# Performance work log

Hardware: AMD Instinct MI355X
Metric: run time of the kernel (lower is better)

## Reference

```python
import jax, jax.numpy as jnp
import numpy as np

# SDNet-CTRL cfg constants
MU = 0.1          # FISTA step size (cfg['MODEL']['MU'])
LMBD = 0.1        # sparsity weight (cfg['MODEL']['LAMBDA'][0])
N_STEPS = 4       # FISTA iterations (cfg['MODEL']['NUM_LAYERS'])
EPS_BN = 1e-5


def _conv(x, w, stride, padding):
    # torch F.conv2d, NCHW / OIHW
    return jax.lax.conv_general_dilated(
        x, w, window_strides=(stride, stride),
        padding=[(padding, padding), (padding, padding)],
        dimension_numbers=('NCHW', 'OIHW', 'NCHW'))


def _conv_t(c, w, stride, padding):
    # torch F.conv_transpose2d(c, w, stride, padding) with output_padding chosen
    # so that it exactly inverts the spatial map of _conv (k=4,s=2,p=1 -> 0).
    k = w.shape[2]
    w_t = jnp.flip(w, (2, 3)).transpose(1, 0, 2, 3)  # (I,O,k,k) flipped
    pad = k - 1 - padding
    return jax.lax.conv_general_dilated(
        c, w_t, window_strides=(1, 1),
        padding=[(pad, pad), (pad, pad)],
        lhs_dilation=(stride, stride),
        dimension_numbers=('NCHW', 'OIHW', 'NCHW'))


def _shrink_nn(c, thr):
    # non-negative soft threshold (cfg NONEGATIVE=True)
    return jax.nn.relu(c - thr)


def _dict_conv(x, w, stride, padding):
    # DictBlock: FISTA convolutional sparse coding, n_dict=1, w_norm=True.
    # normalize each dictionary atom (output filter) to unit l2 norm
    wn = w * jax.lax.rsqrt(jnp.sum(w * w, axis=(1, 2, 3), keepdims=True))
    ss = MU
    thr = LMBD * ss
    # t = 0
    c = _shrink_nn(ss * _conv(x, wn, stride, padding), thr)
    c_pre_pre = jnp.zeros_like(c)
    c_pre = c
    tk = 1.0
    for t in range(1, N_STEPS):
        tk_pre = tk
        tk = (1.0 + float(np.sqrt(1.0 + 4.0 * tk_pre * tk_pre))) / 2.0
        y = c_pre + ((tk_pre - 1.0) / tk) * (c_pre - c_pre_pre)
        r = x - _conv_t(y, wn, stride, padding)      # residual in image space
        c = _shrink_nn(y + ss * _conv(r, wn, stride, padding), thr)
        c_pre_pre, c_pre = c_pre, c
    return c


def _bn(x, g, b):
    # training-mode BatchNorm2d (batch statistics)
    m = jnp.mean(x, axis=(0, 2, 3), keepdims=True)
    v = jnp.var(x, axis=(0, 2, 3), keepdims=True)
    return g.reshape(1, -1, 1, 1) * (x - m) * jax.lax.rsqrt(v + EPS_BN) + b.reshape(1, -1, 1, 1)


def _lrelu(x):
    return jnp.where(x >= 0, x, 0.2 * x)


def setup_inputs() -> dict:
    key = jax.random.key(0)
    ks = jax.random.split(key, 5)
    nc, ndf, nz = 3, 128, 256
    B, H = 256, 32

    def mk_w(k, o, i):
        return jax.random.normal(k, (o, i, 4, 4), jnp.float32) * 0.02

    return {
        'x': jax.random.normal(ks[0], (B, nc, H, H), jnp.float32),
        'w1': mk_w(ks[1], ndf, nc),
        'w2': mk_w(ks[2], 2 * ndf, ndf),
        'w3': mk_w(ks[3], 4 * ndf, 2 * ndf),
        'w4': mk_w(ks[4], nz, 4 * ndf),
        'g2': jnp.ones((2 * ndf,), jnp.float32),
        'b2': jnp.zeros((2 * ndf,), jnp.float32),
        'g3': jnp.ones((4 * ndf,), jnp.float32),
        'b3': jnp.zeros((4 * ndf,), jnp.float32),
    }


def reference(x, w1, w2, w3, w4, g2, b2, g3, b3):
    h = _lrelu(_dict_conv(x, w1, 2, 1))                 # (B, ndf, 16, 16)
    h = _lrelu(_bn(_dict_conv(h, w2, 2, 1), g2, b2))    # (B, 2ndf, 8, 8)
    h = _lrelu(_bn(_dict_conv(h, w3, 2, 1), g3, b3))    # (B, 4ndf, 4, 4)
    h = _dict_conv(h, w4, 1, 0)                         # (B, nz, 1, 1)
    h = h.reshape(h.shape[0], -1)                       # Flatten
    n = jnp.sqrt(jnp.sum(h * h, axis=1, keepdims=True))
    return h / jnp.maximum(n, 1e-12)                    # F.normalize(dim=1)
```

## Files before the change

kernel.cpp:

```cpp
#include <hip/hip_runtime.h>
#include <math.h>

#define SS   0.1f
#define THRC 0.01f

typedef __attribute__((ext_vector_type(8))) short s16x8;
typedef __attribute__((ext_vector_type(4))) float f32x4;

__device__ __forceinline__ float b2f(unsigned short u){
  union{unsigned int i; float f;} v; v.i = ((unsigned int)u)<<16; return v.f;
}
__device__ __forceinline__ unsigned short f2b(float f){
  union{float f; unsigned int i;} v; v.f = f;
  return (unsigned short)((v.i + 0x7fffu + ((v.i>>16)&1u))>>16);
}
__device__ __forceinline__ s16x8 as_s16x8(uint4 u){
  union{uint4 a; s16x8 b;} c; c.a = u; return c.b;
}
__device__ __forceinline__ int swz8(int row, int q){ return (row<<3) | (q ^ (row&7)); }

__device__ __forceinline__ void gld16(const void* g, void* l){
  __builtin_amdgcn_global_load_lds(
      (const __attribute__((address_space(1))) unsigned int*)g,
      (__attribute__((address_space(3))) unsigned int*)l, 16, 0, 0);
}

enum { EPI_FIRST=0, EPI_UPDATE=1, EPI_PARTIAL=2, EPI_RES_NHWC=3, EPI_RES_FLAT=4 };

struct EpiM {
  unsigned short* C;
  const unsigned short* Y;
  const unsigned short* Cprev;
  unsigned short* Yout;
  const unsigned short* img;
  const unsigned short* zp;
  float coef;
  int lH, lW, lC;
  int S_MN, Kc;
};

struct LA_ident {
  const unsigned short* A; int K;
  __device__ void setz(int){}
  __device__ __forceinline__ const unsigned short* addr(int m, int k8) const {
    return A + (size_t)m*K + ((size_t)k8<<3);
  }
};
struct LA_nhwc {
  const unsigned short* img; const unsigned short* zp; int lH, lW, lC;
  __device__ void setz(int){}
  __device__ __forceinline__ const unsigned short* addr(int m, int k8) const {
    int lWo = lW-1, lHo = lH-1;
    int wo = m & ((1<<lWo)-1); int t = m>>lWo; int ho = t & ((1<<lHo)-1); int b = t>>lHo;
    int k = k8<<3; int kk = k>>lC; int i = k & ((1<<lC)-1);
    int kw = kk&3, kh = kk>>2;
    int h = 2*ho + kh - 1, w = 2*wo + kw - 1;
    if ((unsigned)h >= (1u<<lH) || (unsigned)w >= (1u<<lW)) return zp;
    return img + (((((((size_t)b<<lH)|h)<<lW)|w))<<lC) + i;
  }
};
struct LA_yg {
  const unsigned short* y; const unsigned short* zp; int lHo, lWo, lO, ph, pw;
  __device__ void setz(int z){ ph = z>>1; pw = z&1; }
  __device__ __forceinline__ const unsigned short* addr(int m, int k8) const {
    int l = m & ((1<<lWo)-1); int t = m>>lWo; int j = t & ((1<<lHo)-1); int b = t>>lHo;
    int k = k8<<3; int tt = k>>lO; int o = k & ((1<<lO)-1);
    int th = tt>>1, tw = tt&1;
    int ho = ph ? (j+1-th) : (j-th);
    int wo = pw ? (l+1-tw) : (l-tw);
    if ((unsigned)ho >= (1u<<lHo) || (unsigned)wo >= (1u<<lWo)) return zp;
    return y + (((((((size_t)b<<lHo)|ho)<<lWo)|wo))<<lO) + o;
  }
};
struct LA_padb {
  const unsigned short* img;
  __device__ void setz(int){}
  __device__ __forceinline__ const unsigned short* addr(int m, int k8) const {
    int wo = m&15, t = m>>4, ho = t&15, b = t>>4;
    int kh = k8>>1, kw0 = (k8&1)<<1;
    int h = 2*ho + kh, w = 2*wo + kw0;
    return img + (((size_t)b*34 + h)*34 + w)*4;
  }
};

template<class AL, int EPI>
__global__ __launch_bounds__(512)
void mgemm_k(AL al, const unsigned short* __restrict__ Bw, int M, int N, int K, EpiM ep)
{
  __shared__ uint4 S[2][2048];
  const int tid = threadIdx.x;
  const int bm = blockIdx.y<<7, bn = blockIdx.x<<7;
  const int z = blockIdx.z;
  int kb = 0, ke = K;
  const unsigned short* Bp = Bw;
  if (EPI == EPI_PARTIAL){ kb = z*ep.Kc; ke = kb + ep.Kc; }
  if (EPI == EPI_RES_NHWC){ Bp = Bw + (size_t)z*(size_t)N*K; al.setz(z); }

  f32x4 acc[4][2];
  #pragma unroll
  for (int i=0;i<4;++i)
    #pragma unroll
    for (int j=0;j<2;++j){ acc[i][j][0]=0.f; acc[i][j][1]=0.f; acc[i][j][2]=0.f; acc[i][j][3]=0.f; }

  const int lane = tid & 63, wid = tid >> 6;
  const int wm = (wid>>2)<<6, wn = (wid&3)<<5;
  const int fr = lane & 15, fq = lane >> 4;

  auto issue = [&](int k0, int b){
    int k8 = k0>>3;
    #pragma unroll
    for (int i=0;i<2;++i){
      int s  = (wid<<7) + (i<<6) + lane;
      int sr = s>>3, q = (s&7) ^ (sr&7);
      gld16(al.addr(bm+sr, k8+q), (void*)&S[b][(wid<<7) + (i<<6)]);
    }
    #pragma unroll
    for (int i=0;i<2;++i){
      int s  = (wid<<7) + (i<<6) + lane;
      int sr = s>>3, q = (s&7) ^ (sr&7);
      int gn = bn + sr;
      const unsigned short* src = (gn < N) ? Bp + (size_t)gn*K + ((size_t)(k8+q)<<3) : ep.zp;
      gld16(src, (void*)&S[b][1024 + (wid<<7) + (i<<6)]);
    }
  };

  issue(kb, 0);
  int buf = 0;
  for (int k0 = kb; k0 < ke; k0 += 64){
    asm volatile("s_waitcnt vmcnt(0)" ::: "memory");
    __builtin_amdgcn_s_barrier();
    __builtin_amdgcn_sched_barrier(0);
    if (k0 + 64 < ke) issue(k0 + 64, buf^1);
    const uint4* As = &S[buf][0];
    const uint4* Bs = &S[buf][1024];
    #pragma unroll
    for (int half=0; half<2; ++half){
      const int qb = (half<<2) | fq;
      s16x8 af[4], bf[2];
      #pragma unroll
      for (int mi=0;mi<4;++mi) af[mi] = as_s16x8(As[swz8(wm + mi*16 + fr, qb)]);
      #pragma unroll
      for (int ni=0;ni<2;++ni) bf[ni] = as_s16x8(Bs[swz8(wn + ni*16 + fr, qb)]);
      #pragma unroll
      for (int mi=0;mi<4;++mi)
        #pragma unroll
        for (int ni=0;ni<2;++ni)
          acc[mi][ni] = __builtin_amdgcn_mfma_f32_16x16x32_bf16(af[mi], bf[ni], acc[mi][ni], 0,0,0);
    }
    buf ^= 1;
  }

  #pragma unroll
  for (int mi=0;mi<4;++mi){
    #pragma unroll
    for (int ni=0;ni<2;++ni){
      int n = bn + wn + ni*16 + fr;
      if (n >= N) continue;
      int mb = bm + wm + mi*16 + (fq<<2);
      #pragma unroll
      for (int r=0;r<4;++r){
        int m = mb + r;
        float a = acc[mi][ni][r];
        if (EPI == EPI_FIRST){
          float v = SS*a - THRC; v = v>0.f ? v : 0.f;
          ep.C[(size_t)m*N + n] = f2b(v);
        } else if (EPI == EPI_UPDATE){
          size_t idx = (size_t)m*N + n;
          float v = b2f(ep.Y[idx]) + SS*a - THRC; v = v>0.f ? v : 0.f;
          ep.C[idx] = f2b(v);
          if (ep.Yout) ep.Yout[idx] = f2b(v + ep.coef*(v - b2f(ep.Cprev[idx])));
        } else if (EPI == EPI_PARTIAL){
          ep.C[(size_t)z*ep.S_MN + (size_t)m*N + n] = f2b(a);
        } else if (EPI == EPI_RES_NHWC){
          int lWo = ep.lW-1, lHo = ep.lH-1;
          int l = m & ((1<<lWo)-1); int t = m>>lWo; int j = t & ((1<<lHo)-1); int b = t>>lHo;
          int h = 2*j + (z>>1), w = 2*l + (z&1);
          size_t ridx = (((((((size_t)b<<ep.lH)|h)<<ep.lW)|w))<<ep.lC) | n;
          ep.C[ridx] = f2b(b2f(ep.img[ridx]) - a);
        } else {
          size_t ridx = (size_t)m*N + n;
          ep.C[ridx] = f2b(b2f(ep.img[ridx]) - a);
        }
      }
    }
  }
}

__global__ __launch_bounds__(64)
void wnorm1_k(const float* __restrict__ w, unsigned short* __restrict__ wf1,
              unsigned short* __restrict__ wcolT)
{
  int o = blockIdx.x, tid = threadIdx.x;
  __shared__ float red[64];
  float v = (tid < 48) ? w[(size_t)o*48 + tid] : 0.f;
  red[tid] = v*v; __syncthreads();
  for (int d=32; d>0; d>>=1){ if (tid<d) red[tid] += red[tid+d]; __syncthreads(); }
  float nv = v * rsqrtf(red[0]);
  if (tid < 48){
    int c = tid>>4, t = tid&15;
    wf1[(size_t)o*64 + t*4 + c] = f2b(nv);
    wcolT[(size_t)(t*4+c)*128 + o] = f2b(nv);
  } else {
    int t = tid - 48;
    wf1[(size_t)o*64 + t*4 + 3] = 0;
    wcolT[(size_t)(t*4+3)*128 + o] = 0;
  }
}
__global__ __launch_bounds__(256)
void wnormX_k(const float* __restrict__ w, int Cin, int O,
              unsigned short* __restrict__ wT, unsigned short* __restrict__ wclsT,
              unsigned short* __restrict__ wEO)
{
  int o = blockIdx.x, tid = threadIdx.x; int E = Cin*16;
  __shared__ float red[256];
  float s = 0.f;
  for (int e = tid; e < E; e += 256){ float v = w[(size_t)o*E + e]; s += v*v; }
  red[tid] = s; __syncthreads();
  for (int d=128; d>0; d>>=1){ if (tid<d) red[tid] += red[tid+d]; __syncthreads(); }
  float scale = rsqrtf(red[0]);
  for (int e = tid; e < E; e += 256){
    float v = w[(size_t)o*E + e] * scale;
    int i = e>>4, t = e&15, kh = t>>2, kw = t&3;
    int ee = t*Cin + i;
    if (wT)  wT[(size_t)o*E + ee] = f2b(v);
    if (wEO) wEO[(size_t)ee*O + o] = f2b(v);
    if (wclsT){
      int ph = (kh&1)^1, pw = (kw&1)^1, cls = ph*2+pw;
      int tt = (kh>>1)*2 + (kw>>1);
      wclsT[(((size_t)cls*Cin + i)*4 + tt)*O + o] = f2b(v);
    }
  }
}

__global__ void splitk_shrink_k(const unsigned short* __restrict__ part,
                                const unsigned short* __restrict__ Y,
                                unsigned short* __restrict__ C,
                                unsigned short* __restrict__ Yout,
                                const unsigned short* __restrict__ Cprev,
                                float coef, int MN, int S)
{
  for (int i = blockIdx.x*blockDim.x + threadIdx.x; i < MN; i += gridDim.x*blockDim.x){
    float s = 0.f;
    for (int zz = 0; zz < S; ++zz) s += b2f(part[(size_t)zz*MN + i]);
    float v = (Y ? b2f(Y[i]) : 0.f) + SS*s - THRC; v = v>0.f ? v : 0.f;
    C[i] = f2b(v);
    if (Yout) Yout[i] = f2b(v + coef*(v - b2f(Cprev[i])));
  }
}

__global__ void pad_x_k(const float* __restrict__ x, unsigned short* __restrict__ xpb){
  int idx = blockIdx.x*256 + threadIdx.x;
  if (idx >= 262144) return;
  int w = idx&31, t = idx>>5, h = t&31, b = t>>5;
  size_t src = (size_t)b*3072 + h*32 + w;
  unsigned short* d = xpb + (((size_t)b*34 + h+1)*34 + w+1)*4;
  d[0] = f2b(x[src]); d[1] = f2b(x[src+1024]); d[2] = f2b(x[src+2048]); d[3] = 0;
}

__global__ void l1_resid_k(const unsigned short* __restrict__ Col,
                           const float* __restrict__ x, unsigned short* __restrict__ r1pb)
{
  int idx = blockIdx.x*256 + threadIdx.x;
  if (idx >= 262144) return;
  int w = idx&31, t = idx>>5, h = t&31, b = t>>5;
  float a0=0.f, a1=0.f, a2=0.f;
  #pragma unroll
  for (int kh=0; kh<4; ++kh){
    int hh = h+1-kh; if (hh & 1) continue; int ho = hh>>1; if ((unsigned)ho >= 16u) continue;
    #pragma unroll
    for (int kw=0; kw<4; ++kw){
      int ww = w+1-kw; if (ww & 1) continue; int wo = ww>>1; if ((unsigned)wo >= 16u) continue;
      int m = (b*16+ho)*16+wo;
      const unsigned short* cp = Col + (size_t)m*64 + (kh*4+kw)*4;
      a0 += b2f(cp[0]); a1 += b2f(cp[1]); a2 += b2f(cp[2]);
    }
  }
  size_t src = (size_t)b*3072 + h*32 + w;
  unsigned short* d = r1pb + (((size_t)b*34 + h+1)*34 + w+1)*4;
  d[0] = f2b(x[src] - a0); d[1] = f2b(x[src+1024] - a1); d[2] = f2b(x[src+2048] - a2); d[3] = 0;
}

__global__ void bn_stats_k(const unsigned short* __restrict__ d, float* __restrict__ sums,
                           int rows, int O){
  for (int c = threadIdx.x; c < O; c += blockDim.x){
    float a = 0.f, b = 0.f;
    for (int r = blockIdx.x; r < rows; r += gridDim.x){
      float v = b2f(d[(size_t)r*O + c]); a += v; b += v*v;
    }
    atomicAdd(&sums[c], a); atomicAdd(&sums[O+c], b);
  }
}
__global__ void bn_apply_k(const unsigned short* __restrict__ d, const float* __restrict__ sums,
                           const float* __restrict__ g, const float* __restrict__ bta,
                           unsigned short* __restrict__ outp, int rows, int O, float inv_cnt){
  int total = rows*O;
  for (int i = blockIdx.x*blockDim.x + threadIdx.x; i < total; i += gridDim.x*blockDim.x){
    int c = i % O;
    float mean = sums[c]*inv_cnt;
    float var  = sums[O+c]*inv_cnt - mean*mean;
    float v = g[c]*(b2f(d[i])-mean)*rsqrtf(var + 1e-5f) + bta[c];
    outp[i] = f2b(v >= 0.f ? v : 0.2f*v);
  }
}

__global__ __launch_bounds__(256)
void norm_rows_k(const unsigned short* __restrict__ h, float* __restrict__ out){
  int row = blockIdx.x, tid = threadIdx.x;
  __shared__ float red[256];
  float v = b2f(h[(size_t)row*256 + tid]);
  red[tid] = v*v; __syncthreads();
  for (int d=128; d>0; d>>=1){ if (tid<d) red[tid] += red[tid+d]; __syncthreads(); }
  float nrm = sqrtf(red[0]); nrm = nrm > 1e-12f ? nrm : 1e-12f;
  out[(size_t)row*256 + tid] = v / nrm;
}

extern "C" void kernel_launch(void* const* d_in, const int* in_sizes, int n_in,
                              void* d_out, int out_size, void* d_ws, size_t ws_size,
                              hipStream_t stream)
{
  const float* x  = (const float*)d_in[0];
  const float* w1 = (const float*)d_in[1];
  const float* w2 = (const float*)d_in[2];
  const float* w3 = (const float*)d_in[3];
  const float* w4 = (const float*)d_in[4];
  const float* g2 = (const float*)d_in[5];
  const float* b2 = (const float*)d_in[6];
  const float* g3 = (const float*)d_in[7];
  const float* b3 = (const float*)d_in[8];
  float* out = (float*)d_out;

  char* p = (char*)d_ws;
  auto ah = [&](size_t n){ unsigned short* r = (unsigned short*)p; p += n*2; return r; };
  auto af = [&](size_t n){ float* r = (float*)p; p += n*4; return r; };

  unsigned short* wf1    = ah(128*64);
  unsigned short* wcol1T = ah(64*128);
  unsigned short* wT2    = ah((size_t)256*2048);
  unsigned short* wcls2  = ah((size_t)4*128*1024);
  unsigned short* wT3    = ah((size_t)512*4096);
  unsigned short* wcls3  = ah((size_t)4*256*2048);
  unsigned short* wT4    = ah((size_t)256*8192);
  unsigned short* wE4    = ah((size_t)8192*256);
  unsigned short* h1     = ah((size_t)8388608);
  unsigned short* h2     = ah((size_t)4194304);
  unsigned short* h3     = ah((size_t)2097152);
  unsigned short* cA     = ah((size_t)8388608);
  unsigned short* cB     = ah((size_t)8388608);
  unsigned short* yA     = ah((size_t)8388608);
  unsigned short* yB     = ah((size_t)8388608);
  unsigned short* rH     = ah((size_t)8388608);
  char* regionA = p; p += 17858560;
  unsigned short* Col    = (unsigned short*)regionA;
  unsigned short* xpb    = (unsigned short*)(regionA + 8388608);
  unsigned short* r1pb   = (unsigned short*)(regionA + 8388608 + 2367488);
  unsigned short* partL3 = (unsigned short*)regionA;
  unsigned short* partL4 = (unsigned short*)regionA;
  float* bnsum = af(1024);
  unsigned short* zp16 = ah(128);

  double tk = 1.0; float coef[4] = {0.f,0.f,0.f,0.f};
  for (int t = 1; t < 4; ++t){
    double tkp = tk; tk = (1.0 + sqrt(1.0 + 4.0*tkp*tkp))*0.5;
    coef[t] = (float)((tkp - 1.0)/tk);
  }

  hipMemsetAsync(zp16, 0, 256, stream);
  hipMemsetAsync(xpb,  0, 2367488, stream);
  hipMemsetAsync(r1pb, 0, 2367488, stream);
  pad_x_k<<<1024,256,0,stream>>>(x, xpb);
  wnorm1_k<<<128, 64, 0, stream>>>(w1, wf1, wcol1T);
  wnormX_k<<<256,256,0,stream>>>(w2, 128, 256, wT2, wcls2, nullptr);
  wnormX_k<<<512,256,0,stream>>>(w3, 256, 512, wT3, wcls3, nullptr);
  wnormX_k<<<256,256,0,stream>>>(w4, 512, 256, wT4, nullptr, wE4);

  auto l1_fwd = [&](const unsigned short* src, const unsigned short* Y, const unsigned short* Cp,
                    unsigned short* Cout, unsigned short* Yout, float cf){
    LA_padb al{src};
    EpiM ep{}; ep.C=Cout; ep.Y=Y; ep.Cprev=Cp; ep.Yout=Yout; ep.coef=cf; ep.zp=zp16;
    dim3 g(1, 512, 1);
    if (Y) mgemm_k<LA_padb,EPI_UPDATE><<<g,512,0,stream>>>(al, wf1, 65536,128,64, ep);
    else   mgemm_k<LA_padb,EPI_FIRST ><<<g,512,0,stream>>>(al, wf1, 65536,128,64, ep);
  };
  auto l1_tconv = [&](const unsigned short* y){
    LA_ident al{y, 128};
    EpiM ep{}; ep.C=Col; ep.S_MN=0; ep.Kc=128; ep.zp=zp16;
    mgemm_k<LA_ident,EPI_PARTIAL><<<dim3(1,512,1),512,0,stream>>>(al, wcol1T, 65536,64,128, ep);
    l1_resid_k<<<1024,256,0,stream>>>(Col, x, r1pb);
  };
  l1_fwd(xpb,  nullptr, nullptr, cA, nullptr, 0.f);
  l1_tconv(cA);
  l1_fwd(r1pb, cA, cA, cB, yA, coef[2]);
  l1_tconv(yA);
  l1_fwd(r1pb, yA, cB, cA, yB, coef[3]);
  l1_tconv(yB);
  l1_fwd(r1pb, yB, nullptr, h1, nullptr, 0.f);

  auto l2_fwd = [&](const unsigned short* src, const unsigned short* Y, const unsigned short* Cp,
                    unsigned short* Cout, unsigned short* Yout, float cf){
    LA_nhwc al{src, zp16, 4,4,7};
    EpiM ep{}; ep.C=Cout; ep.Y=Y; ep.Cprev=Cp; ep.Yout=Yout; ep.coef=cf; ep.zp=zp16;
    dim3 g(2, 128, 1);
    if (Y) mgemm_k<LA_nhwc,EPI_UPDATE><<<g,512,0,stream>>>(al, wT2, 16384,256,2048, ep);
    else   mgemm_k<LA_nhwc,EPI_FIRST ><<<g,512,0,stream>>>(al, wT2, 16384,256,2048, ep);
  };
  auto l2_tconv = [&](const unsigned short* y){
    LA_yg al{y, zp16, 3,3,8, 0,0};
    EpiM ep{}; ep.C=rH; ep.img=h1; ep.lH=4; ep.lW=4; ep.lC=7; ep.zp=zp16;
    mgemm_k<LA_yg,EPI_RES_NHWC><<<dim3(1,128,4),512,0,stream>>>(al, wcls2, 16384,128,1024, ep);
  };
  l2_fwd(h1, nullptr, nullptr, cA, nullptr, 0.f);
  l2_tconv(cA);
  l2_fwd(rH, cA, cA, cB, yA, coef[2]);
  l2_tconv(yA);
  l2_fwd(rH, yA, cB, cA, yB, coef[3]);
  l2_tconv(yB);
  l2_fwd(rH, yB, nullptr, cB, nullptr, 0.f);
  hipMemsetAsync(bnsum, 0, 2*256*sizeof(float), stream);
  bn_stats_k<<<256,256,0,stream>>>(cB, bnsum, 16384, 256);
  bn_apply_k<<<2048,256,0,stream>>>(cB, bnsum, g2, b2, h2, 16384, 256, 1.f/16384.f);

  auto l3_fwd = [&](const unsigned short* src, const unsigned short* Y, const unsigned short* Cp,
                    unsigned short* Cout, unsigned short* Yout, float cf){
    LA_nhwc al{src, zp16, 3,3,8};
    EpiM ep{}; ep.C=partL3; ep.S_MN=4096*512; ep.Kc=1024; ep.zp=zp16;
    mgemm_k<LA_nhwc,EPI_PARTIAL><<<dim3(4,32,4),512,0,stream>>>(al, wT3, 4096,512,4096, ep);
    splitk_shrink_k<<<1024,256,0,stream>>>(partL3, Y, Cout, Yout, Cp, cf, 4096*512, 4);
  };
  auto l3_tconv = [&](const unsigned short* y){
    LA_yg al{y, zp16, 2,2,9, 0,0};
    EpiM ep{}; ep.C=rH; ep.img=h2; ep.lH=3; ep.lW=3; ep.lC=8; ep.zp=zp16;
    mgemm_k<LA_yg,EPI_RES_NHWC><<<dim3(2,32,4),512,0,stream>>>(al, wcls3, 4096,256,2048, ep);
  };
  l3_fwd(h2, nullptr, nullptr, cA, nullptr, 0.f);
  l3_tconv(cA);
  l3_fwd(rH, cA, cA, cB, yA, coef[2]);
  l3_tconv(yA);
  l3_fwd(rH, yA, cB, cA, yB, coef[3]);
  l3_tconv(yB);
  l3_fwd(rH, yB, nullptr, cB, nullptr, 0.f);
  hipMemsetAsync(bnsum, 0, 2*512*sizeof(float), stream);
  bn_stats_k<<<256,256,0,stream>>>(cB, bnsum, 4096, 512);
  bn_apply_k<<<2048,256,0,stream>>>(cB, bnsum, g3, b3, h3, 4096, 512, 1.f/4096.f);

  auto l4_fwd = [&](const unsigned short* Asrc, const unsigned short* Y, const unsigned short* Cp,
                    unsigned short* Cout, unsigned short* Yout, float cf){
    LA_ident al{Asrc, 8192};
    EpiM ep{}; ep.C=partL4; ep.S_MN=65536; ep.Kc=256; ep.zp=zp16;
    mgemm_k<LA_ident,EPI_PARTIAL><<<dim3(2,2,32),512,0,stream>>>(al, wT4, 256,256,8192, ep);
    splitk_shrink_k<<<256,256,0,stream>>>(partL4, Y, Cout, Yout, Cp, cf, 65536, 32);
  };
  auto l4_tconv = [&](const unsigned short* y){
    LA_ident al{y, 256};
    EpiM ep{}; ep.C=rH; ep.img=h3; ep.zp=zp16;
    mgemm_k<LA_ident,EPI_RES_FLAT><<<dim3(64,2,1),512,0,stream>>>(al, wE4, 256,8192,256, ep);
  };
  l4_fwd(h3, nullptr, nullptr, cA, nullptr, 0.f);
  l4_tconv(cA);
  l4_fwd(rH, cA, cA, cB, yA, coef[2]);
  l4_tconv(yA);
  l4_fwd(rH, yA, cB, cA, yB, coef[3]);
  l4_tconv(yB);
  l4_fwd(rH, yB, nullptr, cB, nullptr, 0.f);

  norm_rows_k<<<256,256,0,stream>>>(cB, out);
}
```

Measured before the change: 889.3 us.

## Split-K layers 2-3 forward and transposed convs, single-buffer LDS, vectorize reductions

Moves the layer-2 forward GEMM and the layer-2/3 transposed-conv GEMMs to split-K with bf16 partial buffers, adds a tcomb kernel to reduce them and subtract from the image, and deepens split-K for layers 3 and 4. The GEMM kernel drops double-buffered LDS for a single buffer with load-then-barrier, halving LDS per block to raise occupancy at the cost of losing load/compute overlap. The split-K shrink reduction is vectorized to 16-byte loads. The aim is more blocks for small grids on many CUs, paid for with extra partial-sum memory traffic, extra launches, and bf16 rounding of partials.

```diff
diff --git a/kernel.cpp b/kernel.cpp
--- a/kernel.cpp
+++ b/kernel.cpp
@@ -25,7 +25,7 @@
       (__attribute__((address_space(3))) unsigned int*)l, 16, 0, 0);
 }
 
-enum { EPI_FIRST=0, EPI_UPDATE=1, EPI_PARTIAL=2, EPI_RES_NHWC=3, EPI_RES_FLAT=4 };
+enum { EPI_FIRST=0, EPI_UPDATE=1, EPI_PARTIAL=2, EPI_TPART=3, EPI_RES_FLAT=4 };
 
 struct EpiM {
   unsigned short* C;
@@ -35,8 +35,7 @@
   const unsigned short* img;
   const unsigned short* zp;
   float coef;
-  int lH, lW, lC;
-  int S_MN, Kc;
+  int S_MN, Kc, lgS;
 };
 
 struct LA_ident {
@@ -87,14 +86,19 @@
 __global__ __launch_bounds__(512)
 void mgemm_k(AL al, const unsigned short* __restrict__ Bw, int M, int N, int K, EpiM ep)
 {
-  __shared__ uint4 S[2][2048];
+  __shared__ uint4 As[1024];
+  __shared__ uint4 Bs[1024];
   const int tid = threadIdx.x;
   const int bm = blockIdx.y<<7, bn = blockIdx.x<<7;
   const int z = blockIdx.z;
   int kb = 0, ke = K;
   const unsigned short* Bp = Bw;
   if (EPI == EPI_PARTIAL){ kb = z*ep.Kc; ke = kb + ep.Kc; }
-  if (EPI == EPI_RES_NHWC){ Bp = Bw + (size_t)z*(size_t)N*K; al.setz(z); }
+  if (EPI == EPI_TPART){
+    int cls = z >> ep.lgS, kz = z & ((1<<ep.lgS)-1);
+    Bp = Bw + (size_t)cls*(size_t)N*K; al.setz(cls);
+    kb = kz*ep.Kc; ke = kb + ep.Kc;
+  }
 
   f32x4 acc[4][2];
   #pragma unroll
@@ -106,33 +110,32 @@
   const int wm = (wid>>2)<<6, wn = (wid&3)<<5;
   const int fr = lane & 15, fq = lane >> 4;
 
-  auto issue = [&](int k0, int b){
+  auto issueA = [&](int k0){
     int k8 = k0>>3;
     #pragma unroll
     for (int i=0;i<2;++i){
       int s  = (wid<<7) + (i<<6) + lane;
       int sr = s>>3, q = (s&7) ^ (sr&7);
-      gld16(al.addr(bm+sr, k8+q), (void*)&S[b][(wid<<7) + (i<<6)]);
-    }
+      gld16(al.addr(bm+sr, k8+q), (void*)&As[(wid<<7) + (i<<6)]);
+    }
+  };
+  auto issueB = [&](int k0){
+    int k8 = k0>>3;
     #pragma unroll
     for (int i=0;i<2;++i){
       int s  = (wid<<7) + (i<<6) + lane;
       int sr = s>>3, q = (s&7) ^ (sr&7);
       int gn = bn + sr;
       const unsigned short* src = (gn < N) ? Bp + (size_t)gn*K + ((size_t)(k8+q)<<3) : ep.zp;
-      gld16(src, (void*)&S[b][1024 + (wid<<7) + (i<<6)]);
-    }
-  };
-
-  issue(kb, 0);
-  int buf = 0;
+      gld16(src, (void*)&Bs[(wid<<7) + (i<<6)]);
+    }
+  };
+
   for (int k0 = kb; k0 < ke; k0 += 64){
+    issueA(k0); issueB(k0);
     asm volatile("s_waitcnt vmcnt(0)" ::: "memory");
     __builtin_amdgcn_s_barrier();
     __builtin_amdgcn_sched_barrier(0);
-    if (k0 + 64 < ke) issue(k0 + 64, buf^1);
-    const uint4* As = &S[buf][0];
-    const uint4* Bs = &S[buf][1024];
     #pragma unroll
     for (int half=0; half<2; ++half){
       const int qb = (half<<2) | fq;
@@ -147,7 +150,10 @@
         for (int ni=0;ni<2;++ni)
           acc[mi][ni] = __builtin_amdgcn_mfma_f32_16x16x32_bf16(af[mi], bf[ni], acc[mi][ni], 0,0,0);
     }
-    buf ^= 1;
+    if (k0 + 64 < ke){
+      __builtin_amdgcn_s_barrier();
+      __builtin_amdgcn_sched_barrier(0);
+    }
   }
 
   #pragma unroll
@@ -169,14 +175,8 @@
           float v = b2f(ep.Y[idx]) + SS*a - THRC; v = v>0.f ? v : 0.f;
           ep.C[idx] = f2b(v);
           if (ep.Yout) ep.Yout[idx] = f2b(v + ep.coef*(v - b2f(ep.Cprev[idx])));
-        } else if (EPI == EPI_PARTIAL){
+        } else if (EPI == EPI_PARTIAL || EPI == EPI_TPART){
           ep.C[(size_t)z*ep.S_MN + (size_t)m*N + n] = f2b(a);
-        } else if (EPI == EPI_RES_NHWC){
-          int lWo = ep.lW-1, lHo = ep.lH-1;
-          int l = m & ((1<<lWo)-1); int t = m>>lWo; int j = t & ((1<<lHo)-1); int b = t>>lHo;
-          int h = 2*j + (z>>1), w = 2*l + (z&1);
-          size_t ridx = (((((((size_t)b<<ep.lH)|h)<<ep.lW)|w))<<ep.lC) | n;
-          ep.C[ridx] = f2b(b2f(ep.img[ridx]) - a);
         } else {
           size_t ridx = (size_t)m*N + n;
           ep.C[ridx] = f2b(b2f(ep.img[ridx]) - a);
@@ -239,12 +239,65 @@
                                 const unsigned short* __restrict__ Cprev,
                                 float coef, int MN, int S)
 {
-  for (int i = blockIdx.x*blockDim.x + threadIdx.x; i < MN; i += gridDim.x*blockDim.x){
-    float s = 0.f;
-    for (int zz = 0; zz < S; ++zz) s += b2f(part[(size_t)zz*MN + i]);
-    float v = (Y ? b2f(Y[i]) : 0.f) + SS*s - THRC; v = v>0.f ? v : 0.f;
-    C[i] = f2b(v);
-    if (Yout) Yout[i] = f2b(v + coef*(v - b2f(Cprev[i])));
+  int total8 = MN>>3;
+  for (int i8 = blockIdx.x*blockDim.x + threadIdx.x; i8 < total8; i8 += gridDim.x*blockDim.x){
+    size_t off = (size_t)i8<<3;
+    float s[8];
+    #pragma unroll
+    for (int j=0;j<8;++j) s[j]=0.f;
+    for (int zz = 0; zz < S; ++zz){
+      uint4 pv = *(const uint4*)(part + (size_t)zz*MN + off);
+      const unsigned short* pe = (const unsigned short*)&pv;
+      #pragma unroll
+      for (int j=0;j<8;++j) s[j] += b2f(pe[j]);
+    }
+    uint4 yv = make_uint4(0,0,0,0), cp = make_uint4(0,0,0,0);
+    if (Y)    yv = *(const uint4*)(Y + off);
+    if (Yout) cp = *(const uint4*)(Cprev + off);
+    const unsigned short* ye = (const unsigned short*)&yv;
+    const unsigned short* ce = (const unsigned short*)&cp;
+    unsigned short co[8], yo[8];
+    #pragma unroll
+    for (int j=0;j<8;++j){
+      float v = (Y ? b2f(ye[j]) : 0.f) + SS*s[j] - THRC; v = v>0.f ? v : 0.f;
+      co[j] = f2b(v);
+      if (Yout) yo[j] = f2b(v + coef*(v - b2f(ce[j])));
+    }
+    *(uint4*)(C + off) = *(const uint4*)co;
+    if (Yout) *(uint4*)(Yout + off) = *(const uint4*)yo;
+  }
+}
+
+__global__ void tcomb_k(const unsigned short* __restrict__ part,
+                        const unsigned short* __restrict__ img,
+                        unsigned short* __restrict__ outp,
+                        int lH, int lW, int lC, int S, int MN, int total8)
+{
+  for (int i8 = blockIdx.x*blockDim.x + threadIdx.x; i8 < total8; i8 += gridDim.x*blockDim.x){
+    size_t idx = (size_t)i8<<3;
+    int c = (int)(idx & ((1u<<lC)-1));
+    int w = (int)(idx>>lC) & ((1<<lW)-1);
+    int h = (int)(idx>>(lC+lW)) & ((1<<lH)-1);
+    int b = (int)(idx>>(lC+lW+lH));
+    int j = h>>1, l = w>>1, cls = ((h&1)<<1)|(w&1);
+    int m = (((b<<(lH-1))|j)<<(lW-1))|l;
+    int N = 1<<lC;
+    const unsigned short* pb = part + ((size_t)cls*S)*MN + (size_t)m*N + c;
+    float s[8];
+    #pragma unroll
+    for (int q=0;q<8;++q) s[q]=0.f;
+    for (int kz=0; kz<S; ++kz){
+      uint4 pv = *(const uint4*)(pb + (size_t)kz*MN);
+      const unsigned short* pe = (const unsigned short*)&pv;
+      #pragma unroll
+      for (int q=0;q<8;++q) s[q] += b2f(pe[q]);
+    }
+    uint4 iv = *(const uint4*)(img + idx);
+    const unsigned short* ie = (const unsigned short*)&iv;
+    unsigned short ro[8];
+    #pragma unroll
+    for (int q=0;q<8;++q) ro[q] = f2b(b2f(ie[q]) - s[q]);
+    *(uint4*)(outp + idx) = *(const uint4*)ro;
   }
 }
 
@@ -349,12 +402,11 @@
   unsigned short* yA     = ah((size_t)8388608);
   unsigned short* yB     = ah((size_t)8388608);
   unsigned short* rH     = ah((size_t)8388608);
-  char* regionA = p; p += 17858560;
+  char* regionA = p; p += 33554432;
   unsigned short* Col    = (unsigned short*)regionA;
   unsigned short* xpb    = (unsigned short*)(regionA + 8388608);
   unsigned short* r1pb   = (unsigned short*)(regionA + 8388608 + 2367488);
-  unsigned short* partL3 = (unsigned short*)regionA;
-  unsigned short* partL4 = (unsigned short*)regionA;
+  unsigned short* partB  = (unsigned short*)regionA;
   float* bnsum = af(1024);
   unsigned short* zp16 = ah(128);
 
@@ -398,15 +450,15 @@
   auto l2_fwd = [&](const unsigned short* src, const unsigned short* Y, const unsigned short* Cp,
                     unsigned short* Cout, unsigned short* Yout, float cf){
     LA_nhwc al{src, zp16, 4,4,7};
-    EpiM ep{}; ep.C=Cout; ep.Y=Y; ep.Cprev=Cp; ep.Yout=Yout; ep.coef=cf; ep.zp=zp16;
-    dim3 g(2, 128, 1);
-    if (Y) mgemm_k<LA_nhwc,EPI_UPDATE><<<g,512,0,stream>>>(al, wT2, 16384,256,2048, ep);
-    else   mgemm_k<LA_nhwc,EPI_FIRST ><<<g,512,0,stream>>>(al, wT2, 16384,256,2048, ep);
+    EpiM ep{}; ep.C=partB; ep.S_MN=16384*256; ep.Kc=512; ep.zp=zp16;
+    mgemm_k<LA_nhwc,EPI_PARTIAL><<<dim3(2,128,4),512,0,stream>>>(al, wT2, 16384,256,2048, ep);
+    splitk_shrink_k<<<2048,256,0,stream>>>(partB, Y, Cout, Yout, Cp, cf, 16384*256, 4);
   };
   auto l2_tconv = [&](const unsigned short* y){
     LA_yg al{y, zp16, 3,3,8, 0,0};
-    EpiM ep{}; ep.C=rH; ep.img=h1; ep.lH=4; ep.lW=4; ep.lC=7; ep.zp=zp16;
-    mgemm_k<LA_yg,EPI_RES_NHWC><<<dim3(1,128,4),512,0,stream>>>(al, wcls2, 16384,128,1024, ep);
+    EpiM ep{}; ep.C=partB; ep.S_MN=16384*128; ep.Kc=512; ep.lgS=1; ep.zp=zp16;
+    mgemm_k<LA_yg,EPI_TPART><<<dim3(1,128,8),512,0,stream>>>(al, wcls2, 16384,128,1024, ep);
+    tcomb_k<<<2048,256,0,stream>>>(partB, h1, rH, 4,4,7, 2, 16384*128, 1048576);
   };
   l2_fwd(h1, nullptr, nullptr, cA, nullptr, 0.f);
   l2_tconv(cA);
@@ -422,14 +474,15 @@
   auto l3_fwd = [&](const unsigned short* src, const unsigned short* Y, const unsigned short* Cp,
                     unsigned short* Cout, unsigned short* Yout, float cf){
     LA_nhwc al{src, zp16, 3,3,8};
-    EpiM ep{}; ep.C=partL3; ep.S_MN=4096*512; ep.Kc=1024; ep.zp=zp16;
-    mgemm_k<LA_nhwc,EPI_PARTIAL><<<dim3(4,32,4),512,0,stream>>>(al, wT3, 4096,512,4096, ep);
-    splitk_shrink_k<<<1024,256,0,stream>>>(partL3, Y, Cout, Yout, Cp, cf, 4096*512, 4);
+    EpiM ep{}; ep.C=partB; ep.S_MN=4096*512; ep.Kc=512; ep.zp=zp16;
+    mgemm_k<LA_nhwc,EPI_PARTIAL><<<dim3(4,32,8),512,0,stream>>>(al, wT3, 4096,512,4096, ep);
+    splitk_shrink_k<<<1024,256,0,stream>>>(partB, Y, Cout, Yout, Cp, cf, 4096*512, 8);
   };
   auto l3_tconv = [&](const unsigned short* y){
     LA_yg al{y, zp16, 2,2,9, 0,0};
-    EpiM ep{}; ep.C=rH; ep.img=h2; ep.lH=3; ep.lW=3; ep.lC=8; ep.zp=zp16;
-    mgemm_k<LA_yg,EPI_RES_NHWC><<<dim3(2,32,4),512,0,stream>>>(al, wcls3, 4096,256,2048, ep);
+    EpiM ep{}; ep.C=partB; ep.S_MN=4096*256; ep.Kc=512; ep.lgS=2; ep.zp=zp16;
+    mgemm_k<LA_yg,EPI_TPART><<<dim3(2,32,16),512,0,stream>>>(al, wcls3, 4096,256,2048, ep);
+    tcomb_k<<<2048,256,0,stream>>>(partB, h2, rH, 3,3,8, 4, 4096*256, 524288);
   };
   l3_fwd(h2, nullptr, nullptr, cA, nullptr, 0.f);
   l3_tconv(cA);
@@ -445,9 +498,9 @@
   auto l4_fwd = [&](const unsigned short* Asrc, const unsigned short* Y, const unsigned short* Cp,
                     unsigned short* Cout, unsigned short* Yout, float cf){
     LA_ident al{Asrc, 8192};
-    EpiM ep{}; ep.C=partL4; ep.S_MN=65536; ep.Kc=256; ep.zp=zp16;
-    mgemm_k<LA_ident,EPI_PARTIAL><<<dim3(2,2,32),512,0,stream>>>(al, wT4, 256,256,8192, ep);
-    splitk_shrink_k<<<256,256,0,stream>>>(partL4, Y, Cout, Yout, Cp, cf, 65536, 32);
+    EpiM ep{}; ep.C=partB; ep.S_MN=65536; ep.Kc=128; ep.zp=zp16;
+    mgemm_k<LA_ident,EPI_PARTIAL><<<dim3(2,2,64),512,0,stream>>>(al, wT4, 256,256,8192, ep);
+    splitk_shrink_k<<<32,256,0,stream>>>(partB, Y, Cout, Yout, Cp, cf, 65536, 64);
   };
   auto l4_tconv = [&](const unsigned short* y){
     LA_ident al{y, 256};
```

Measured after the change: 912.4 us. +2.6%, slower.
